# Kernel optimization log

Measured on AMD Instinct MI355X. Metric: run time of the kernel, lower is better.

Reference implementation:

```python
import jax, jax.numpy as jnp
import numpy as np

CHUNK = 32
NUM_HEADS = 4
HEAD_K = 256
HEAD_V = 256
EPS = 1e-05


def l2norm(x, eps=1e-6):
    return x * jax.lax.rsqrt(jnp.sum(x * x, axis=-1, keepdims=True) + eps)


def causal_depthwise_conv(x, w):
    # x: [b, l, d], w: [d, K]; causal depthwise conv1d (left pad K-1)
    K = w.shape[1]
    l = x.shape[1]
    xp = jnp.pad(x, ((0, 0), (K - 1, 0), (0, 0)))
    return sum(w[:, k] * xp[:, k:k + l, :] for k in range(K))


def delta_rule_chunkwise(q, k, v, beta):
    # q,k: [b,h,l,dk], v: [b,h,l,dv], beta: [b,h,l]; l divisible by CHUNK
    b, h, l, dk = q.shape
    dv = v.shape[-1]
    c = CHUNK
    n = l // c
    q = l2norm(q)
    k = l2norm(k)
    v = v * beta[..., None]
    k_beta = k * beta[..., None]
    resh = lambda x: x.reshape(b, h, n, c, x.shape[-1])
    q, k, v, k_beta = map(resh, (q, k, v, k_beta))
    tri_strict = jnp.tril(jnp.ones((c, c), dtype=q.dtype), -1)  # strictly lower
    attn = -(k_beta @ jnp.swapaxes(k, -1, -2)) * tri_strict  # [b,h,n,c,c]

    def body(i, a):
        # a[i, :i] += sum_j a[i, j] * a[j, :i]; zero elsewhere by structure
        row = a[..., i, :]  # [b,h,n,c]
        upd = jnp.einsum('bhnj,bhnjk->bhnk', row, a)
        return a.at[..., i, :].add(upd)

    attn = jax.lax.fori_loop(1, c, body, attn)
    attn = attn + jnp.eye(c, dtype=attn.dtype)
    u = attn @ v        # [b,h,n,c,dv]
    w = attn @ k_beta   # [b,h,n,c,dk]

    mask_causal = jnp.tril(jnp.ones((c, c), dtype=q.dtype), 0)  # incl diag
    S0 = jnp.zeros((b, h, dk, dv), dtype=q.dtype)
    to_front = lambda x: jnp.moveaxis(x, 2, 0)  # [n,b,h,c,d]

    def step(S, inp):
        q_i, k_i, u_i, w_i = inp
        attn_i = (q_i @ jnp.swapaxes(k_i, -1, -2)) * mask_causal
        u_new = u_i - w_i @ S
        o_i = q_i @ S + attn_i @ u_new
        S = S + jnp.swapaxes(k_i, -1, -2) @ u_new
        return S, o_i

    S, o = jax.lax.scan(step, S0, (to_front(q), to_front(k), to_front(u), to_front(w)))
    o = jnp.moveaxis(o, 0, 2).reshape(b, h, l, dv)
    return o, S


def setup_inputs() -> dict:
    key = jax.random.key(0)
    ks = jax.random.split(key, 12)
    b, l, d = 4, 4096, 1024
    sc = 0.02
    return {
        'hidden_states': jax.random.normal(ks[0], (b, l, d), jnp.float32),
        'Wq': jax.random.normal(ks[1], (1024, 1024), jnp.float32) * sc,
        'Wk': jax.random.normal(ks[2], (1024, 1024), jnp.float32) * sc,
        'Wv': jax.random.normal(ks[3], (1024, 1024), jnp.float32) * sc,
        'conv_q': jax.random.normal(ks[4], (1024, 4), jnp.float32) * 0.1,
        'conv_k': jax.random.normal(ks[5], (1024, 4), jnp.float32) * 0.1,
        'conv_v': jax.random.normal(ks[6], (1024, 4), jnp.float32) * 0.1,
        'Wb': jax.random.normal(ks[7], (4, 1024), jnp.float32) * sc,
        'Wmix': jax.random.normal(ks[8], (4, 1024), jnp.float32) * sc,
        'norm_w': jnp.ones((256,), jnp.float32),
        'Wo': jax.random.normal(ks[9], (1024, 1024), jnp.float32) * sc,
    }


def reference(hidden_states, Wq, Wk, Wv, conv_q, conv_k, conv_v, Wb, Wmix, norm_w, Wo):
    x = hidden_states
    b, l, d = x.shape
    h, dk, dv = NUM_HEADS, HEAD_K, HEAD_V
    # projections + depthwise causal short conv + silu
    q = jax.nn.silu(causal_depthwise_conv(x @ Wq.T, conv_q))
    k = jax.nn.silu(causal_depthwise_conv(x @ Wk.T, conv_k))
    v = jax.nn.silu(causal_depthwise_conv(x @ Wv.T, conv_v))
    v_token = v.reshape(b, l, h, dv)
    qh = q.reshape(b, l, h, dk).transpose(0, 2, 1, 3)
    kh = k.reshape(b, l, h, dk).transpose(0, 2, 1, 3)
    vh = v_token.transpose(0, 2, 1, 3)
    beta = jax.nn.sigmoid(x @ Wb.T).transpose(0, 2, 1)  # [b,h,l]
    o, S = delta_rule_chunkwise(qh, kh, vh, beta)
    o = o.transpose(0, 2, 1, 3)  # [b,l,h,dv]
    mix = jax.nn.sigmoid(x @ Wmix.T)[..., None]  # [b,l,h,1]
    o = mix * o + (1.0 - mix) * v_token
    # per-head RMSNorm
    o = o * jax.lax.rsqrt(jnp.mean(o * o, axis=-1, keepdims=True) + EPS) * norm_w
    o = o.reshape(b, l, h * dv) @ Wo.T
    return o
```

## Files before the change

### kernel.cpp

```cpp
#include <hip/hip_runtime.h>
#include <hip/hip_bf16.h>

typedef __hip_bfloat16 bf16;
typedef unsigned short u16;
typedef __attribute__((ext_vector_type(4))) float f32x4;
typedef __attribute__((ext_vector_type(8))) short bf16x8;
typedef __attribute__((ext_vector_type(2))) unsigned int u32x2;

#define MFMA16(a, b, c) __builtin_amdgcn_mfma_f32_16x16x32_bf16((a), (b), (c), 0, 0, 0)

__device__ __forceinline__ float bfu2f(u16 u){
  return __uint_as_float(((unsigned int)u) << 16);
}
__device__ __forceinline__ u16 f2bfu(float x){
  return __builtin_bit_cast(u16, __float2bfloat16(x));
}
__device__ __forceinline__ void gload16(const void* g, const void* l){
  __builtin_amdgcn_global_load_lds(
      (const __attribute__((address_space(1))) unsigned int*)g,
      (__attribute__((address_space(3))) unsigned int*)l, 16, 0, 0);
}

__global__ __launch_bounds__(256) void cvt_bf16(
    const float* __restrict__ src, u16* __restrict__ dst, int n8)
{
  int i = blockIdx.x * 256 + threadIdx.x;
  if (i >= n8) return;
  const float4* s = (const float4*)src;
  float4 a = s[i * 2], b = s[i * 2 + 1];
  u16 o[8] = {f2bfu(a.x), f2bfu(a.y), f2bfu(a.z), f2bfu(a.w),
              f2bfu(b.x), f2bfu(b.y), f2bfu(b.z), f2bfu(b.w)};
  *(bf16x8*)(dst + (size_t)i * 8) = *(bf16x8*)o;
}

__global__ __launch_bounds__(256) void cvt3_bf16(
    const float* __restrict__ s0, const float* __restrict__ s1, const float* __restrict__ s2,
    u16* __restrict__ d0, u16* __restrict__ d1, u16* __restrict__ d2)
{
  const float* s; u16* d;
  if (blockIdx.y == 0)      { s = s0; d = d0; }
  else if (blockIdx.y == 1) { s = s1; d = d1; }
  else                      { s = s2; d = d2; }
  int i = blockIdx.x * 256 + threadIdx.x;
  const float4* sp = (const float4*)s;
  float4 a = sp[i * 2], b = sp[i * 2 + 1];
  u16 o[8] = {f2bfu(a.x), f2bfu(a.y), f2bfu(a.z), f2bfu(a.w),
              f2bfu(b.x), f2bfu(b.y), f2bfu(b.z), f2bfu(b.w)};
  *(bf16x8*)(d + (size_t)i * 8) = *(bf16x8*)o;
}

template<int NMAT, bool F32OUT>
__global__ __launch_bounds__(256) void gemm_bt(
    const u16* __restrict__ A,
    const u16* __restrict__ B0, const u16* __restrict__ B1, const u16* __restrict__ B2,
    void* __restrict__ C0, void* __restrict__ C1, void* __restrict__ C2)
{
  const u16* B; void* C;
  if (NMAT == 1 || blockIdx.z == 0){ B = B0; C = C0; }
  else if (blockIdx.z == 1)        { B = B1; C = C1; }
  else                             { B = B2; C = C2; }
  __shared__ char lds[2][2][16384];
  const int tid = threadIdx.x;
  const int lane = tid & 63, wv = tid >> 6;
  const int lc = lane & 15, lh = lane >> 4;
  const int wr = wv >> 1, wc = wv & 1;
  const int lin = blockIdx.x + (blockIdx.y << 7);
  const int m0 = ((lin & 7) * 16 + (lin >> 6)) * 128;
  const int n0 = ((lin >> 3) & 7) * 128;

  f32x4 acc[4][4];
  #pragma unroll
  for (int mt = 0; mt < 4; mt++)
    #pragma unroll
    for (int nt = 0; nt < 4; nt++) acc[mt][nt] = (f32x4){0.f, 0.f, 0.f, 0.f};

  auto stage = [&](int buf, int k0){
    #pragma unroll
    for (int c = 0; c < 4; c++){
      const int q = wv * 4096 + c * 1024;
      const int row = (q >> 7) + (lane >> 3);
      const int slot = (lane & 7) ^ (row & 7);
      gload16(A + (size_t)(m0 + row) * 1024 + k0 + slot * 8, &lds[buf][0][q]);
      gload16(B + (size_t)(n0 + row) * 1024 + k0 + slot * 8, &lds[buf][1][q]);
    }
  };

  stage(0, 0);
  __syncthreads();
  int cur = 0;
  for (int t = 0; t < 16; t++){
    if (t < 15) stage(cur ^ 1, (t + 1) * 64);
    const char* Abuf = lds[cur][0];
    const char* Bbuf = lds[cur][1];
    #pragma unroll
    for (int kk = 0; kk < 2; kk++){
      bf16x8 af[4], bfr[4];
      #pragma unroll
      for (int mt = 0; mt < 4; mt++){
        int r = wr * 64 + mt * 16 + lc;
        int slot = (kk * 4 + lh) ^ (r & 7);
        af[mt] = *(const bf16x8*)(const void*)(Abuf + r * 128 + slot * 16);
      }
      #pragma unroll
      for (int nt = 0; nt < 4; nt++){
        int r = wc * 64 + nt * 16 + lc;
        int slot = (kk * 4 + lh) ^ (r & 7);
        bfr[nt] = *(const bf16x8*)(const void*)(Bbuf + r * 128 + slot * 16);
      }
      #pragma unroll
      for (int mt = 0; mt < 4; mt++)
        #pragma unroll
        for (int nt = 0; nt < 4; nt++)
          acc[mt][nt] = MFMA16(af[mt], bfr[nt], acc[mt][nt]);
    }
    __syncthreads();
    cur ^= 1;
  }

  #pragma unroll
  for (int mt = 0; mt < 4; mt++)
    #pragma unroll
    for (int nt = 0; nt < 4; nt++)
      #pragma unroll
      for (int rg = 0; rg < 4; rg++){
        int row = m0 + wr * 64 + mt * 16 + lh * 4 + rg;
        int col = n0 + wc * 64 + nt * 16 + lc;
        if (F32OUT) ((float*)C)[(size_t)row * 1024 + col] = acc[mt][nt][rg];
        else ((bf16*)C)[(size_t)row * 1024 + col] = __float2bfloat16(acc[mt][nt][rg]);
      }
}

__global__ __launch_bounds__(256) void small_proj(
    const float* __restrict__ x, const float* __restrict__ Wb,
    const float* __restrict__ Wmix, float* __restrict__ beta, float* __restrict__ mixb)
{
  const int tok = blockIdx.x;
  const int tid = threadIdx.x;
  __shared__ __align__(16) float xrow[1024];
  ((float4*)xrow)[tid] = ((const float4*)(x + (size_t)tok * 1024))[tid];
  __syncthreads();
  const int o = tid >> 5, g = tid & 31;
  const float* Wrow = (o < 4) ? (Wb + (size_t)o * 1024) : (Wmix + (size_t)(o - 4) * 1024);
  float p = 0.f;
  for (int e = g; e < 256; e += 32){
    float4 xv = ((const float4*)xrow)[e];
    float4 wv = ((const float4*)Wrow)[e];
    p += xv.x * wv.x + xv.y * wv.y + xv.z * wv.z + xv.w * wv.w;
  }
  for (int off = 16; off; off >>= 1) p += __shfl_down(p, off, 32);
  if (g == 0){
    float s = 1.f / (1.f + expf(-p));
    int b = tok >> 12, t = tok & 4095;
    if (o < 4) beta[((size_t)(b * 4 + o)) * 4096 + t] = s;
    else       mixb[(size_t)tok * 4 + (o - 4)] = s;
  }
}

__global__ __launch_bounds__(256) void conv_silu3(
    const bf16* __restrict__ in0, const bf16* __restrict__ in1, const bf16* __restrict__ in2,
    const float* __restrict__ w0, const float* __restrict__ w1, const float* __restrict__ w2,
    bf16* __restrict__ o0, bf16* __restrict__ o1, bf16* __restrict__ o2)
{
  const bf16* in; const float* wc; bf16* out;
  if (blockIdx.y == 0)      { in = in0; wc = w0; out = o0; }
  else if (blockIdx.y == 1) { in = in1; wc = w1; out = o1; }
  else                      { in = in2; wc = w2; out = o2; }
  const int idx8 = blockIdx.x * 256 + threadIdx.x;
  const int c8 = (idx8 & 127) * 8;
  const int tt = idx8 >> 7;
  const int t  = tt & 4095;
  const u16* inu = (const u16*)in;
  const size_t base = (size_t)tt * 1024 + c8;
  bf16x8 zv = {0, 0, 0, 0, 0, 0, 0, 0};
  bf16x8 x3 = *(const bf16x8*)(const void*)(inu + base);
  bf16x8 x2 = (t >= 1) ? *(const bf16x8*)(const void*)(inu + base - 1024) : zv;
  bf16x8 x1 = (t >= 2) ? *(const bf16x8*)(const void*)(inu + base - 2048) : zv;
  bf16x8 x0 = (t >= 3) ? *(const bf16x8*)(const void*)(inu + base - 3072) : zv;
  u16 o8[8];
  #pragma unroll
  for (int e = 0; e < 8; e++){
    const float4 w4 = ((const float4*)wc)[c8 + e];
    float s = w4.w * bfu2f((u16)x3[e]) + w4.z * bfu2f((u16)x2[e])
            + w4.y * bfu2f((u16)x1[e]) + w4.x * bfu2f((u16)x0[e]);
    s = s / (1.f + expf(-s));
    o8[e] = f2bfu(s);
  }
  *(bf16x8*)(void*)((u16*)out + base) = *(bf16x8*)o8;
}

__global__ __launch_bounds__(256, 2) void chunk_prep(
    bf16* __restrict__ qc, const bf16* __restrict__ kc, const bf16* __restrict__ vc,
    const float* __restrict__ beta,
    bf16* __restrict__ u_out, bf16* __restrict__ w_out,
    bf16* __restrict__ Ab, bf16* __restrict__ kTg)
{
  __shared__ char kS[16384], qS[16384];
  __shared__ float att[1056];
  __shared__ char Th[2048], Tl[2048];
  __shared__ char vTh[8192], vTl[8192];
  __shared__ char wTh[8192], wTl[8192];
  __shared__ float rnk_s[32], rnq_s[32], bvec[32];

  const int g = blockIdx.x;
  const int ch = g & 127, h = (g >> 7) & 3, b = g >> 9;
  const int tid = threadIdx.x;
  const int l = tid & 63, wv = tid >> 6;
  const int lc = l & 15, lh = l >> 4;
  const int i = tid >> 3, s = tid & 7;
  const size_t rowbase = ((size_t)(b * 4096 + ch * 32)) * 1024 + (size_t)h * 256;
  const u16* kcu = (const u16*)kc;
  const u16* qcu = (const u16*)qc;
  const u16* vcu = (const u16*)vc;

  bf16x8 kr[4], qr[4], vr[4];
  float ssk = 0.f, ssq = 0.f;
  #pragma unroll
  for (int j4 = 0; j4 < 4; j4++){
    size_t eo = rowbase + (size_t)i * 1024 + s * 32 + j4 * 8;
    kr[j4] = *(const bf16x8*)(const void*)(kcu + eo);
    qr[j4] = *(const bf16x8*)(const void*)(qcu + eo);
    vr[j4] = *(const bf16x8*)(const void*)(vcu + eo);
    #pragma unroll
    for (int e = 0; e < 8; e++){
      float kv = bfu2f((u16)kr[j4][e]); ssk += kv * kv;
      float qv = bfu2f((u16)qr[j4][e]); ssq += qv * qv;
    }
  }
  #pragma unroll
  for (int off = 1; off < 8; off <<= 1){
    ssk += __shfl_xor(ssk, off, 64);
    ssq += __shfl_xor(ssq, off, 64);
  }
  if (s == 0){
    rnk_s[i] = 1.0f / sqrtf(ssk + 1e-6f);
    rnq_s[i] = 1.0f / sqrtf(ssq + 1e-6f);
  }
  if (tid < 32) bvec[tid] = beta[((size_t)(b * 4 + h)) * 4096 + ch * 32 + tid];
  __syncthreads();

  const float rk = rnk_s[i], rq = rnq_s[i], bi = bvec[i];
  #pragma unroll
  for (int j4 = 0; j4 < 4; j4++){
    u16 kn8[8], qn8[8];
    #pragma unroll
    for (int e = 0; e < 8; e++){
      kn8[e] = f2bfu(bfu2f((u16)kr[j4][e]) * rk);
      qn8[e] = f2bfu(bfu2f((u16)qr[j4][e]) * rq);
    }
    int byt = (i * 512 + s * 64 + j4 * 16) ^ ((i & 7) << 4);
    *(bf16x8*)(void*)(kS + byt) = *(bf16x8*)kn8;
    *(bf16x8*)(void*)(qS + byt) = *(bf16x8*)qn8;
    *(bf16x8*)(void*)((u16*)qc + rowbase + (size_t)i * 1024 + s * 32 + j4 * 8) = *(bf16x8*)kn8 * 0 + *(bf16x8*)qn8;
  }
  if ((s >> 2) == 0){
    #pragma unroll
    for (int j4 = 0; j4 < 4; j4++)
      #pragma unroll
      for (int e = 0; e < 8; e++){
        int dl = (s & 3) * 32 + j4 * 8 + e;
        float vb = bfu2f((u16)vr[j4][e]) * bi;
        float kb = bfu2f((u16)kr[j4][e]) * rk * bi;
        u16 vh = f2bfu(vb), kh = f2bfu(kb);
        u16 vlo = f2bfu(vb - bfu2f(vh)), klo = f2bfu(kb - bfu2f(kh));
        int byt = dl * 64 + (((i >> 3) ^ ((dl >> 1) & 3)) << 4) + (i & 7) * 2;
        *(u16*)(vTh + byt) = vh; *(u16*)(vTl + byt) = vlo;
        *(u16*)(wTh + byt) = kh; *(u16*)(wTl + byt) = klo;
      }
  }
  __syncthreads();

  {
    const int mq = wv >> 1, nq = wv & 1;
    const int rowA = mq * 16 + lc, rowB = nq * 16 + lc;
    const int swA = (rowA & 7) << 4, swB = (rowB & 7) << 4;
    f32x4 accL = (f32x4){0.f, 0.f, 0.f, 0.f};
    f32x4 accA = (f32x4){0.f, 0.f, 0.f, 0.f};
    #pragma unroll
    for (int kt = 0; kt < 8; kt++){
      bf16x8 af  = *(const bf16x8*)(const void*)(kS + ((rowA * 512 + kt * 64 + lh * 16) ^ swA));
      bf16x8 bf_ = *(const bf16x8*)(const void*)(kS + ((rowB * 512 + kt * 64 + lh * 16) ^ swB));
      bf16x8 aq  = *(const bf16x8*)(const void*)(qS + ((rowA * 512 + kt * 64 + lh * 16) ^ swA));
      accL = MFMA16(af, bf_, accL);
      accA = MFMA16(aq, bf_, accA);
    }
    #pragma unroll
    for (int r = 0; r < 4; r++){
      int rr = mq * 16 + lh * 4 + r, cc = nq * 16 + lc;
      att[rr * 33 + cc] = (cc < rr) ? (-bvec[rr] * accL[r]) : 0.f;
      float av = (cc <= rr) ? accA[r] : 0.f;
      ((u16*)Ab)[(size_t)g * 1024 + rr * 32 + cc] = f2bfu(av);
    }
  }
  {
    u16 tmp[32];
    #pragma unroll
    for (int i2 = 0; i2 < 32; i2++)
      tmp[i2] = *(const u16*)(kS + ((i2 * 512 + tid * 2) ^ ((i2 & 7) << 4)));
    #pragma unroll
    for (int j4 = 0; j4 < 4; j4++)
      *(bf16x8*)(void*)((u16*)kTg + (size_t)g * 8192 + tid * 32 + j4 * 8) = *(bf16x8*)(tmp + j4 * 8);
  }
  __syncthreads();

  if (wv == 0 && l < 32){
    for (int ii = 1; ii < 32; ii++){
      float upd = 0.f;
      for (int m = 0; m < ii; m++)
        upd += att[ii * 33 + m] * att[m * 33 + l];
      att[ii * 33 + l] += upd;
    }
    att[l * 33 + l] = 1.0f;
  }
  __syncthreads();

  #pragma unroll
  for (int z = 0; z < 4; z++){
    int e = tid * 4 + z;
    int row = e >> 5, col = e & 31;
    float f = att[row * 33 + col];
    u16 hh = f2bfu(f), llo = f2bfu(f - bfu2f(hh));
    int byt = row * 64 + ((((col >> 3)) ^ ((row >> 1) & 3)) << 4) + (col & 7) * 2;
    *(u16*)(Th + byt) = hh; *(u16*)(Tl + byt) = llo;
  }
  __syncthreads();

  {
    const int mq = wv >> 1, nsel = wv & 1;
    const int rowA = mq * 16 + lc;
    const int sa = (lh ^ ((rowA >> 1) & 3)) << 4;
    bf16x8 ta = *(const bf16x8*)(const void*)(Th + rowA * 64 + sa);
    bf16x8 tl = *(const bf16x8*)(const void*)(Tl + rowA * 64 + sa);
    #pragma unroll
    for (int half = 0; half < 2; half++){
      if (half == 1){
        __syncthreads();
        if ((s >> 2) == 1){
          #pragma unroll
          for (int j4 = 0; j4 < 4; j4++)
            #pragma unroll
            for (int e = 0; e < 8; e++){
              int dl = (s & 3) * 32 + j4 * 8 + e;
              float vb = bfu2f((u16)vr[j4][e]) * bi;
              float kb = bfu2f((u16)kr[j4][e]) * rk * bi;
              u16 vh = f2bfu(vb), kh = f2bfu(kb);
              u16 vlo = f2bfu(vb - bfu2f(vh)), klo = f2bfu(kb - bfu2f(kh));
              int byt = dl * 64 + (((i >> 3) ^ ((dl >> 1) & 3)) << 4) + (i & 7) * 2;
              *(u16*)(vTh + byt) = vh; *(u16*)(vTl + byt) = vlo;
              *(u16*)(wTh + byt) = kh; *(u16*)(wTl + byt) = klo;
            }
        }
        __syncthreads();
      }
      #pragma unroll
      for (int nt = 0; nt < 4; nt++){
        int nl = nsel * 64 + nt * 16;
        int rowB = nl + lc;
        int sb = (lh ^ ((rowB >> 1) & 3)) << 4;
        bf16x8 bh_ = *(const bf16x8*)(const void*)(vTh + rowB * 64 + sb);
        bf16x8 bl_ = *(const bf16x8*)(const void*)(vTl + rowB * 64 + sb);
        f32x4 aU = (f32x4){0.f, 0.f, 0.f, 0.f};
        aU = MFMA16(ta, bh_, aU);
        aU = MFMA16(ta, bl_, aU);
        aU = MFMA16(tl, bh_, aU);
        bf16x8 wh_ = *(const bf16x8*)(const void*)(wTh + rowB * 64 + sb);
        bf16x8 wl_ = *(const bf16x8*)(const void*)(wTl + rowB * 64 + sb);
        f32x4 aW = (f32x4){0.f, 0.f, 0.f, 0.f};
        aW = MFMA16(ta, wh_, aW);
        aW = MFMA16(ta, wl_, aW);
        aW = MFMA16(tl, wh_, aW);
        #pragma unroll
        for (int r = 0; r < 4; r++){
          int row = mq * 16 + lh * 4 + r, col = half * 128 + nl + lc;
          ((u16*)u_out)[rowbase + (size_t)row * 1024 + col] = f2bfu(aU[r]);
          ((u16*)w_out)[rowbase + (size_t)row * 1024 + col] = f2bfu(aW[r]);
        }
      }
    }
  }
}

__global__ __launch_bounds__(128, 1) void scan_kernel(
    const u16* __restrict__ w_in, const u16* __restrict__ qn,
    const u16* __restrict__ u_in, const bf16* __restrict__ Ab,
    const bf16* __restrict__ kTg, bf16* __restrict__ o_out)
{
  extern __shared__ char smem[];
  char* wqbuf  = smem;
  char* stbuf  = smem + 65536;
  char* untbuf = smem + 81920;

  const int tid = threadIdx.x;
  const int l = tid & 63, wv = tid >> 6;
  const int lc = l & 15, lh = l >> 4;
  const int wg = blockIdx.x;
  const int bh = (wg & 7) * 2 + ((wg >> 3) & 1);
  const int vb = wg >> 4;
  const int h = bh & 3, b = bh >> 2;
  const int c0 = vb * 16;
  const int mw = wv * 16;

  f32x4 Sf[8];
  #pragma unroll
  for (int mt = 0; mt < 8; mt++) Sf[mt] = (f32x4){0.f, 0.f, 0.f, 0.f};

  const size_t bhElem = (size_t)b * 4096 * 1024 + (size_t)h * 256;
  const u16* kTu = (const u16*)kTg;

  auto stageWQ = [&](int buf, size_t rowE){
    char* wbase = wqbuf + buf * 32768 + wv * 8192;
    #pragma unroll
    for (int p = 0; p < 8; p++){
      int i = wv * 16 + p * 2 + (l >> 5);
      int logc = (l & 31) ^ (i & 7);
      size_t src = rowE + (size_t)i * 1024 + (size_t)logc * 8;
      gload16(w_in + src, wbase + p * 1024);
      gload16(qn  + src, wbase + 16384 + p * 1024);
    }
  };

  stageWQ(0, bhElem);
  for (int e = tid; e < 4096; e += 128) ((unsigned int*)(void*)stbuf)[e] = 0u;
  u16 cu0 = u_in[bhElem + (size_t)(mw + lh*4 + 0) * 1024 + c0 + lc];
  u16 cu1 = u_in[bhElem + (size_t)(mw + lh*4 + 1) * 1024 + c0 + lc];
  u16 cu2 = u_in[bhElem + (size_t)(mw + lh*4 + 2) * 1024 + c0 + lc];
  u16 cu3 = u_in[bhElem + (size_t)(mw + lh*4 + 3) * 1024 + c0 + lc];
  bf16x8 cAf = *(const bf16x8*)(const void*)(Ab + (size_t)(bh * 128) * 1024 + (mw + lc) * 32 + lh * 8);
  __syncthreads();

  int cur = 0;
  for (int ch = 0; ch < 128; ch++){
    const size_t rowElem = bhElem + (size_t)ch * 32768;
    if (ch < 127) stageWQ(cur ^ 1, rowElem + 32768);
    bf16x8 kF[8];
    {
      const size_t ktCur = (size_t)(bh * 128 + ch) * 8192;
      #pragma unroll
      for (int mt = 0; mt < 8; mt++){
        int rowK = wv * 128 + mt * 16 + lc;
        kF[mt] = *(const bf16x8*)(const void*)(kTu + ktCur + (size_t)rowK * 32 + lh * 8);
      }
    }
    u16 pu0, pu1, pu2, pu3; bf16x8 pAf;
    if (ch < 127){
      const size_t rowN = rowElem + 32768;
      pu0 = u_in[rowN + (size_t)(mw + lh*4 + 0) * 1024 + c0 + lc];
      pu1 = u_in[rowN + (size_t)(mw + lh*4 + 1) * 1024 + c0 + lc];
      pu2 = u_in[rowN + (size_t)(mw + lh*4 + 2) * 1024 + c0 + lc];
      pu3 = u_in[rowN + (size_t)(mw + lh*4 + 3) * 1024 + c0 + lc];
      pAf = *(const bf16x8*)(const void*)(Ab + (size_t)(bh * 128 + ch + 1) * 1024 + (mw + lc) * 32 + lh * 8);
    }

    const char* wl = wqbuf + cur * 32768;
    const char* ql = wl + 16384;

    f32x4 aU0 = (f32x4){0.f,0.f,0.f,0.f}, aU1 = (f32x4){0.f,0.f,0.f,0.f};
    f32x4 aO0 = (f32x4){0.f,0.f,0.f,0.f}, aO1 = (f32x4){0.f,0.f,0.f,0.f};
    {
      const int rowA = mw + lc;
      const int swA = (rowA & 7) << 4;
      const int swS = (lc & 7) << 4;
      #pragma unroll
      for (int kt = 0; kt < 8; kt++){
        const int kb = kt * 64 + lh * 16;
        bf16x8 aw = *(const bf16x8*)(const void*)(wl + ((rowA * 512 + kb) ^ swA));
        bf16x8 aq = *(const bf16x8*)(const void*)(ql + ((rowA * 512 + kb) ^ swA));
        bf16x8 sh = *(const bf16x8*)(const void*)(stbuf + ((lc * 512 + kb) ^ swS));
        bf16x8 sl = *(const bf16x8*)(const void*)(stbuf + 8192 + ((lc * 512 + kb) ^ swS));
        if (kt & 1){
          aU1 = MFMA16(aw, sh, aU1);
          aU1 = MFMA16(aw, sl, aU1);
          aO1 = MFMA16(aq, sh, aO1);
          aO1 = MFMA16(aq, sl, aO1);
        } else {
          aU0 = MFMA16(aw, sh, aU0);
          aU0 = MFMA16(aw, sl, aU0);
          aO0 = MFMA16(aq, sh, aO0);
          aO0 = MFMA16(aq, sl, aO0);
        }
      }
    }
    f32x4 accO = aO0 + aO1;
    {
      f32x4 accU = aU0 + aU1;
      float v0 = bfu2f(cu0) - accU[0];
      float v1 = bfu2f(cu1) - accU[1];
      float v2 = bfu2f(cu2) - accU[2];
      float v3 = bfu2f(cu3) - accU[3];
      u16 h0 = f2bfu(v0), h1 = f2bfu(v1), h2 = f2bfu(v2), h3 = f2bfu(v3);
      u16 l0 = f2bfu(v0 - bfu2f(h0)), l1 = f2bfu(v1 - bfu2f(h1));
      u16 l2 = f2bfu(v2 - bfu2f(h2)), l3 = f2bfu(v3 - bfu2f(h3));
      unsigned int ph0 = (unsigned)h0 | ((unsigned)h1 << 16), ph1 = (unsigned)h2 | ((unsigned)h3 << 16);
      unsigned int pl0 = (unsigned)l0 | ((unsigned)l1 << 16), pl1 = (unsigned)l2 | ((unsigned)l3 << 16);
      int off = lc * 80 + (mw + lh * 4) * 2;
      *(u32x2*)(void*)(untbuf + off)        = (u32x2){ph0, ph1};
      *(u32x2*)(void*)(untbuf + 1280 + off) = (u32x2){pl0, pl1};
    }
    __syncthreads();

    bf16x8 uh = *(const bf16x8*)(const void*)(untbuf + lc * 80 + lh * 16);
    bf16x8 ul = *(const bf16x8*)(const void*)(untbuf + 1280 + lc * 80 + lh * 16);
    accO = MFMA16(cAf, uh, accO);
    accO = MFMA16(cAf, ul, accO);
    o_out[rowElem + (size_t)(mw + lh*4 + 0) * 1024 + c0 + lc] = __float2bfloat16(accO[0]);
    o_out[rowElem + (size_t)(mw + lh*4 + 1) * 1024 + c0 + lc] = __float2bfloat16(accO[1]);
    o_out[rowElem + (size_t)(mw + lh*4 + 2) * 1024 + c0 + lc] = __float2bfloat16(accO[2]);
    o_out[rowElem + (size_t)(mw + lh*4 + 3) * 1024 + c0 + lc] = __float2bfloat16(accO[3]);

    #pragma unroll
    for (int mt = 0; mt < 8; mt++){
      Sf[mt] = MFMA16(kF[mt], uh, Sf[mt]);
      Sf[mt] = MFMA16(kF[mt], ul, Sf[mt]);
    }

    #pragma unroll
    for (int mt = 0; mt < 8; mt++){
      const int dbase = wv * 128 + mt * 16 + lh * 4;
      float v0 = Sf[mt][0], v1 = Sf[mt][1], v2 = Sf[mt][2], v3 = Sf[mt][3];
      u16 h0 = f2bfu(v0), h1 = f2bfu(v1), h2 = f2bfu(v2), h3 = f2bfu(v3);
      u16 s0 = f2bfu(v0 - bfu2f(h0)), s1 = f2bfu(v1 - bfu2f(h1));
      u16 s2 = f2bfu(v2 - bfu2f(h2)), s3 = f2bfu(v3 - bfu2f(h3));
      int off = ((lc * 512 + dbase * 2) ^ ((lc & 7) << 4));
      *(u32x2*)(void*)(stbuf + off) =
          (u32x2){(unsigned)h0 | ((unsigned)h1 << 16), (unsigned)h2 | ((unsigned)h3 << 16)};
      *(u32x2*)(void*)(stbuf + 8192 + off) =
          (u32x2){(unsigned)s0 | ((unsigned)s1 << 16), (unsigned)s2 | ((unsigned)s3 << 16)};
    }
    if (ch < 127){
      cu0 = pu0; cu1 = pu1; cu2 = pu2; cu3 = pu3; cAf = pAf;
    }
    __syncthreads();
    cur ^= 1;
  }
}

__global__ __launch_bounds__(256) void postproc(
    const bf16* __restrict__ o_in, const bf16* __restrict__ v_tok,
    const float* __restrict__ mixb, const float* __restrict__ norm_w,
    bf16* __restrict__ onorm)
{
  const int tid = threadIdx.x;
  const int slot = tid >> 5, g = tid & 31;
  const int blk = blockIdx.x * 8 + slot;
  const size_t base = (size_t)blk * 256 + g * 8;
  const u16* oin = (const u16*)o_in;
  const u16* vin = (const u16*)v_tok;
  bf16x8 ov8 = *(const bf16x8*)(const void*)(oin + base);
  bf16x8 vv8 = *(const bf16x8*)(const void*)(vin + base);
  float m = mixb[blk];
  float val[8];
  float ss = 0.f;
  #pragma unroll
  for (int e = 0; e < 8; e++){
    float v = m * bfu2f((u16)ov8[e]) + (1.f - m) * bfu2f((u16)vv8[e]);
    val[e] = v;
    ss += v * v;
  }
  #pragma unroll
  for (int off = 16; off; off >>= 1) ss += __shfl_down(ss, off, 32);
  ss = __shfl(ss, 0, 32);
  float r = rsqrtf(ss * (1.f / 256.f) + 1e-5f);
  const float4 nw0 = ((const float4*)norm_w)[g * 2];
  const float4 nw1 = ((const float4*)norm_w)[g * 2 + 1];
  const float nw[8] = {nw0.x, nw0.y, nw0.z, nw0.w, nw1.x, nw1.y, nw1.z, nw1.w};
  u16 o8[8];
  #pragma unroll
  for (int e = 0; e < 8; e++) o8[e] = f2bfu(val[e] * r * nw[e]);
  *(bf16x8*)(void*)((u16*)onorm + base) = *(bf16x8*)o8;
}

extern "C" void kernel_launch(void* const* d_in, const int* in_sizes, int n_in,
                              void* d_out, int out_size, void* d_ws, size_t ws_size,
                              hipStream_t stream)
{
  (void)in_sizes; (void)n_in; (void)out_size; (void)ws_size;
  const float* x     = (const float*)d_in[0];
  const float* Wq    = (const float*)d_in[1];
  const float* Wk    = (const float*)d_in[2];
  const float* Wv    = (const float*)d_in[3];
  const float* convq = (const float*)d_in[4];
  const float* convk = (const float*)d_in[5];
  const float* convv = (const float*)d_in[6];
  const float* Wb    = (const float*)d_in[7];
  const float* Wmix  = (const float*)d_in[8];
  const float* normw = (const float*)d_in[9];
  const float* Wo    = (const float*)d_in[10];
  float* out = (float*)d_out;

  char* wsb = (char*)d_ws;
  const size_t BIGB = (size_t)16777216 * 2;
  bf16* b0 = (bf16*)(wsb + 0*BIGB);
  bf16* b1 = (bf16*)(wsb + 1*BIGB);
  bf16* b2 = (bf16*)(wsb + 2*BIGB);
  bf16* b3 = (bf16*)(wsb + 3*BIGB);
  bf16* b4 = (bf16*)(wsb + 4*BIGB);
  bf16* b5 = (bf16*)(wsb + 5*BIGB);
  bf16*  Ab   = (bf16*) (wsb + 6*BIGB);
  float* beta = (float*)(wsb + 6*BIGB + 4194304);
  float* mixb = beta + 65536;
  bf16*  kTg  = (bf16*) (wsb + 6*BIGB + 4194304 + 524288);

  u16* xbf = (u16*)b4;
  u16* wqb = (u16*)b3;
  u16* wkb = wqb + (size_t)1024*1024;
  u16* wvb = wkb + (size_t)1024*1024;
  u16* wob = (u16*)kTg;

  cvt_bf16<<<8192, 256, 0, stream>>>(x, xbf, 2097152);
  cvt3_bf16<<<dim3(512, 3), 256, 0, stream>>>(Wq, Wk, Wv, wqb, wkb, wvb);

  gemm_bt<3, false><<<dim3(128, 8, 3), 256, 0, stream>>>(
      xbf, wqb, wkb, wvb, (void*)b0, (void*)b1, (void*)b2);
  small_proj<<<16384, 256, 0, stream>>>(x, Wb, Wmix, beta, mixb);
  conv_silu3<<<dim3(8192, 3), 256, 0, stream>>>(
      b0, b1, b2, convq, convk, convv, b3, b4, b5);
  chunk_prep<<<2048, 256, 0, stream>>>(b3, b4, b5, beta, b2, b0, Ab, kTg);
  hipFuncSetAttribute((const void*)scan_kernel,
                      hipFuncAttributeMaxDynamicSharedMemorySize, 84480);
  scan_kernel<<<256, 128, 84480, stream>>>((const u16*)b0, (const u16*)b3,
                                           (const u16*)b2, Ab, kTg, b1);
  cvt_bf16<<<512, 256, 0, stream>>>(Wo, wob, 131072);
  postproc  <<<8192, 256, 0, stream>>>(b1, b5, mixb, normw, b3);
  gemm_bt<1, true><<<dim3(128, 8, 1), 256, 0, stream>>>(
      (const u16*)b3, wob, wob, wob, (void*)out, (void*)out, (void*)out);
}
```

Measured before the change: 626.2 us.

## Process chunk pairs in scan with precomputed cross-chunk correction matrices

```diff
diff --git a/kernel.cpp b/kernel.cpp
--- a/kernel.cpp
+++ b/kernel.cpp
@@ -379,10 +379,69 @@
   }
 }
 
+__global__ __launch_bounds__(256) void pair_prep(
+    const u16* __restrict__ w_in, const u16* __restrict__ qn,
+    const bf16* __restrict__ kTg, u16* __restrict__ MN)
+{
+  __shared__ char wS[16384], qS[16384], ktS[16384];
+  const int g2 = blockIdx.x;
+  const int bh = g2 >> 6, p = g2 & 63;
+  const int h = bh & 3, b = bh >> 2;
+  const int tid = threadIdx.x;
+  const int l = tid & 63, wv = tid >> 6;
+  const int lc = l & 15, lh = l >> 4;
+  const int i = tid >> 3, s = tid & 7;
+  const size_t row1 = ((size_t)(b * 4096 + (p * 2 + 1) * 32)) * 1024 + (size_t)h * 256;
+  const u16* kt0 = (const u16*)kTg + (size_t)(bh * 128 + p * 2) * 8192;
+
+  #pragma unroll
+  for (int j4 = 0; j4 < 4; j4++){
+    size_t eo = row1 + (size_t)i * 1024 + s * 32 + j4 * 8;
+    int byt = (i * 512 + s * 64 + j4 * 16) ^ ((i & 7) << 4);
+    *(bf16x8*)(void*)(wS + byt) = *(const bf16x8*)(const void*)(w_in + eo);
+    *(bf16x8*)(void*)(qS + byt) = *(const bf16x8*)(const void*)(qn + eo);
+  }
+  #pragma unroll
+  for (int j = 0; j < 4; j++)
+    *(bf16x8*)(void*)(ktS + tid * 64 + j * 16) = *(const bf16x8*)(const void*)(kt0 + tid * 32 + j * 8);
+  __syncthreads();
+
+  const int mq = wv >> 1, nq = wv & 1;
+  const int rowA = mq * 16 + lc;
+  const int swA = (rowA & 7) << 4;
+  f32x4 accM = (f32x4){0.f, 0.f, 0.f, 0.f};
+  f32x4 accN = (f32x4){0.f, 0.f, 0.f, 0.f};
+  #pragma unroll
+  for (int kt = 0; kt < 8; kt++){
+    bf16x8 aw = *(const bf16x8*)(const void*)(wS + ((rowA * 512 + kt * 64 + lh * 16) ^ swA));
+    bf16x8 aq = *(const bf16x8*)(const void*)(qS + ((rowA * 512 + kt * 64 + lh * 16) ^ swA));
+    u16 bk8[8];
+    #pragma unroll
+    for (int j = 0; j < 8; j++)
+      bk8[j] = *(const u16*)(ktS + (kt * 32 + lh * 8 + j) * 64 + (nq * 16 + lc) * 2);
+    bf16x8 bk = *(bf16x8*)bk8;
+    accM = MFMA16(aw, bk, accM);
+    accN = MFMA16(aq, bk, accN);
+  }
+  u16* base = MN + (size_t)g2 * 4096;
+  #pragma unroll
+  for (int r = 0; r < 4; r++){
+    int rr = mq * 16 + lh * 4 + r, cc = nq * 16 + lc;
+    float m = accM[r], n = accN[r];
+    u16 mh = f2bfu(m), nh = f2bfu(n);
+    u16 ml = f2bfu(m - bfu2f(mh)), nl = f2bfu(n - bfu2f(nh));
+    base[rr * 32 + cc] = mh;
+    base[1024 + rr * 32 + cc] = ml;
+    base[2048 + rr * 32 + cc] = nh;
+    base[3072 + rr * 32 + cc] = nl;
+  }
+}
+
 __global__ __launch_bounds__(128, 1) void scan_kernel(
     const u16* __restrict__ w_in, const u16* __restrict__ qn,
     const u16* __restrict__ u_in, const bf16* __restrict__ Ab,
-    const bf16* __restrict__ kTg, bf16* __restrict__ o_out)
+    const bf16* __restrict__ kTg, const u16* __restrict__ MN,
+    bf16* __restrict__ o_out)
 {
   extern __shared__ char smem[];
   char* wqbuf  = smem;
@@ -409,56 +468,67 @@
   auto stageWQ = [&](int buf, size_t rowE){
     char* wbase = wqbuf + buf * 32768 + wv * 8192;
     #pragma unroll
-    for (int p = 0; p < 8; p++){
-      int i = wv * 16 + p * 2 + (l >> 5);
+    for (int pp = 0; pp < 8; pp++){
+      int i = wv * 16 + pp * 2 + (l >> 5);
       int logc = (l & 31) ^ (i & 7);
       size_t src = rowE + (size_t)i * 1024 + (size_t)logc * 8;
-      gload16(w_in + src, wbase + p * 1024);
-      gload16(qn  + src, wbase + 16384 + p * 1024);
+      gload16(w_in + src, wbase + pp * 1024);
+      gload16(qn  + src, wbase + 16384 + pp * 1024);
     }
   };
 
   stageWQ(0, bhElem);
   for (int e = tid; e < 4096; e += 128) ((unsigned int*)(void*)stbuf)[e] = 0u;
-  u16 cu0 = u_in[bhElem + (size_t)(mw + lh*4 + 0) * 1024 + c0 + lc];
-  u16 cu1 = u_in[bhElem + (size_t)(mw + lh*4 + 1) * 1024 + c0 + lc];
-  u16 cu2 = u_in[bhElem + (size_t)(mw + lh*4 + 2) * 1024 + c0 + lc];
-  u16 cu3 = u_in[bhElem + (size_t)(mw + lh*4 + 3) * 1024 + c0 + lc];
-  bf16x8 cAf = *(const bf16x8*)(const void*)(Ab + (size_t)(bh * 128) * 1024 + (mw + lc) * 32 + lh * 8);
   __syncthreads();
 
   int cur = 0;
-  for (int ch = 0; ch < 128; ch++){
-    const size_t rowElem = bhElem + (size_t)ch * 32768;
-    if (ch < 127) stageWQ(cur ^ 1, rowElem + 32768);
-    bf16x8 kF[8];
+  for (int p = 0; p < 64; p++){
+    const size_t row0 = bhElem + (size_t)(p * 2) * 32768;
+    const size_t row1 = row0 + 32768;
+    if (p < 63) stageWQ(cur ^ 1, row0 + 65536);
+
+    bf16x8 w1f[8], q1f[8];
     {
-      const size_t ktCur = (size_t)(bh * 128 + ch) * 8192;
+      const size_t rowOff1 = row1 + (size_t)(mw + lc) * 1024 + lh * 8;
+      #pragma unroll
+      for (int kt = 0; kt < 8; kt++){
+        w1f[kt] = *(const bf16x8*)(const void*)(w_in + rowOff1 + kt * 32);
+        q1f[kt] = *(const bf16x8*)(const void*)(qn + rowOff1 + kt * 32);
+      }
+    }
+    bf16x8 kF0[8], kF1[8];
+    {
+      const size_t kt0b = (size_t)(bh * 128 + p * 2) * 8192;
       #pragma unroll
       for (int mt = 0; mt < 8; mt++){
         int rowK = wv * 128 + mt * 16 + lc;
-        kF[mt] = *(const bf16x8*)(const void*)(kTu + ktCur + (size_t)rowK * 32 + lh * 8);
-      }
-    }
-    u16 pu0, pu1, pu2, pu3; bf16x8 pAf;
-    if (ch < 127){
-      const size_t rowN = rowElem + 32768;
-      pu0 = u_in[rowN + (size_t)(mw + lh*4 + 0) * 1024 + c0 + lc];
-      pu1 = u_in[rowN + (size_t)(mw + lh*4 + 1) * 1024 + c0 + lc];
-      pu2 = u_in[rowN + (size_t)(mw + lh*4 + 2) * 1024 + c0 + lc];
-      pu3 = u_in[rowN + (size_t)(mw + lh*4 + 3) * 1024 + c0 + lc];
-      pAf = *(const bf16x8*)(const void*)(Ab + (size_t)(bh * 128 + ch + 1) * 1024 + (mw + lc) * 32 + lh * 8);
-    }
+        kF0[mt] = *(const bf16x8*)(const void*)(kTu + kt0b + (size_t)rowK * 32 + lh * 8);
+        kF1[mt] = *(const bf16x8*)(const void*)(kTu + kt0b + 8192 + (size_t)rowK * 32 + lh * 8);
+      }
+    }
+    u16 u0v[4], u1v[4];
+    #pragma unroll
+    for (int r = 0; r < 4; r++){
+      u0v[r] = u_in[row0 + (size_t)(mw + lh*4 + r) * 1024 + c0 + lc];
+      u1v[r] = u_in[row1 + (size_t)(mw + lh*4 + r) * 1024 + c0 + lc];
+    }
+    bf16x8 A0f = *(const bf16x8*)(const void*)(Ab + (size_t)(bh * 128 + p * 2) * 1024 + (mw + lc) * 32 + lh * 8);
+    bf16x8 A1f = *(const bf16x8*)(const void*)(Ab + (size_t)(bh * 128 + p * 2 + 1) * 1024 + (mw + lc) * 32 + lh * 8);
+    const u16* mnb = MN + (size_t)(bh * 64 + p) * 4096;
+    bf16x8 Mhf = *(const bf16x8*)(const void*)(mnb + (mw + lc) * 32 + lh * 8);
+    bf16x8 Mlf = *(const bf16x8*)(const void*)(mnb + 1024 + (mw + lc) * 32 + lh * 8);
+    bf16x8 Nhf = *(const bf16x8*)(const void*)(mnb + 2048 + (mw + lc) * 32 + lh * 8);
+    bf16x8 Nlf = *(const bf16x8*)(const void*)(mnb + 3072 + (mw + lc) * 32 + lh * 8);
 
     const char* wl = wqbuf + cur * 32768;
     const char* ql = wl + 16384;
+    const int swS = (lc & 7) << 4;
 
     f32x4 aU0 = (f32x4){0.f,0.f,0.f,0.f}, aU1 = (f32x4){0.f,0.f,0.f,0.f};
     f32x4 aO0 = (f32x4){0.f,0.f,0.f,0.f}, aO1 = (f32x4){0.f,0.f,0.f,0.f};
     {
       const int rowA = mw + lc;
       const int swA = (rowA & 7) << 4;
-      const int swS = (lc & 7) << 4;
       #pragma unroll
       for (int kt = 0; kt < 8; kt++){
         const int kb = kt * 64 + lh * 16;
@@ -467,49 +537,97 @@
         bf16x8 sh = *(const bf16x8*)(const void*)(stbuf + ((lc * 512 + kb) ^ swS));
         bf16x8 sl = *(const bf16x8*)(const void*)(stbuf + 8192 + ((lc * 512 + kb) ^ swS));
         if (kt & 1){
-          aU1 = MFMA16(aw, sh, aU1);
-          aU1 = MFMA16(aw, sl, aU1);
-          aO1 = MFMA16(aq, sh, aO1);
-          aO1 = MFMA16(aq, sl, aO1);
+          aU1 = MFMA16(aw, sh, aU1); aU1 = MFMA16(aw, sl, aU1);
+          aO1 = MFMA16(aq, sh, aO1); aO1 = MFMA16(aq, sl, aO1);
         } else {
-          aU0 = MFMA16(aw, sh, aU0);
-          aU0 = MFMA16(aw, sl, aU0);
-          aO0 = MFMA16(aq, sh, aO0);
-          aO0 = MFMA16(aq, sl, aO0);
+          aU0 = MFMA16(aw, sh, aU0); aU0 = MFMA16(aw, sl, aU0);
+          aO0 = MFMA16(aq, sh, aO0); aO0 = MFMA16(aq, sl, aO0);
         }
       }
     }
-    f32x4 accO = aO0 + aO1;
+    f32x4 accO0 = aO0 + aO1;
     {
-      f32x4 accU = aU0 + aU1;
-      float v0 = bfu2f(cu0) - accU[0];
-      float v1 = bfu2f(cu1) - accU[1];
-      float v2 = bfu2f(cu2) - accU[2];
-      float v3 = bfu2f(cu3) - accU[3];
+      f32x4 accU0 = aU0 + aU1;
+      float v0 = bfu2f(u0v[0]) - accU0[0];
+      float v1 = bfu2f(u0v[1]) - accU0[1];
+      float v2 = bfu2f(u0v[2]) - accU0[2];
+      float v3 = bfu2f(u0v[3]) - accU0[3];
       u16 h0 = f2bfu(v0), h1 = f2bfu(v1), h2 = f2bfu(v2), h3 = f2bfu(v3);
       u16 l0 = f2bfu(v0 - bfu2f(h0)), l1 = f2bfu(v1 - bfu2f(h1));
       u16 l2 = f2bfu(v2 - bfu2f(h2)), l3 = f2bfu(v3 - bfu2f(h3));
-      unsigned int ph0 = (unsigned)h0 | ((unsigned)h1 << 16), ph1 = (unsigned)h2 | ((unsigned)h3 << 16);
-      unsigned int pl0 = (unsigned)l0 | ((unsigned)l1 << 16), pl1 = (unsigned)l2 | ((unsigned)l3 << 16);
       int off = lc * 80 + (mw + lh * 4) * 2;
-      *(u32x2*)(void*)(untbuf + off)        = (u32x2){ph0, ph1};
-      *(u32x2*)(void*)(untbuf + 1280 + off) = (u32x2){pl0, pl1};
+      *(u32x2*)(void*)(untbuf + off) =
+          (u32x2){(unsigned)h0 | ((unsigned)h1 << 16), (unsigned)h2 | ((unsigned)h3 << 16)};
+      *(u32x2*)(void*)(untbuf + 1280 + off) =
+          (u32x2){(unsigned)l0 | ((unsigned)l1 << 16), (unsigned)l2 | ((unsigned)l3 << 16)};
     }
     __syncthreads();
 
-    bf16x8 uh = *(const bf16x8*)(const void*)(untbuf + lc * 80 + lh * 16);
-    bf16x8 ul = *(const bf16x8*)(const void*)(untbuf + 1280 + lc * 80 + lh * 16);
-    accO = MFMA16(cAf, uh, accO);
-    accO = MFMA16(cAf, ul, accO);
-    o_out[rowElem + (size_t)(mw + lh*4 + 0) * 1024 + c0 + lc] = __float2bfloat16(accO[0]);
-    o_out[rowElem + (size_t)(mw + lh*4 + 1) * 1024 + c0 + lc] = __float2bfloat16(accO[1]);
-    o_out[rowElem + (size_t)(mw + lh*4 + 2) * 1024 + c0 + lc] = __float2bfloat16(accO[2]);
-    o_out[rowElem + (size_t)(mw + lh*4 + 3) * 1024 + c0 + lc] = __float2bfloat16(accO[3]);
-
+    bf16x8 uh0 = *(const bf16x8*)(const void*)(untbuf + lc * 80 + lh * 16);
+    bf16x8 ul0 = *(const bf16x8*)(const void*)(untbuf + 1280 + lc * 80 + lh * 16);
+    accO0 = MFMA16(A0f, uh0, accO0);
+    accO0 = MFMA16(A0f, ul0, accO0);
+    #pragma unroll
+    for (int r = 0; r < 4; r++)
+      o_out[row0 + (size_t)(mw + lh*4 + r) * 1024 + c0 + lc] = __float2bfloat16(accO0[r]);
     #pragma unroll
     for (int mt = 0; mt < 8; mt++){
-      Sf[mt] = MFMA16(kF[mt], uh, Sf[mt]);
-      Sf[mt] = MFMA16(kF[mt], ul, Sf[mt]);
+      Sf[mt] = MFMA16(kF0[mt], uh0, Sf[mt]);
+      Sf[mt] = MFMA16(kF0[mt], ul0, Sf[mt]);
+    }
+
+    f32x4 bU0 = (f32x4){0.f,0.f,0.f,0.f}, bU1 = (f32x4){0.f,0.f,0.f,0.f};
+    f32x4 bO0 = (f32x4){0.f,0.f,0.f,0.f}, bO1 = (f32x4){0.f,0.f,0.f,0.f};
+    {
+      #pragma unroll
+      for (int kt = 0; kt < 8; kt++){
+        const int kb = kt * 64 + lh * 16;
+        bf16x8 sh = *(const bf16x8*)(const void*)(stbuf + ((lc * 512 + kb) ^ swS));
+        bf16x8 sl = *(const bf16x8*)(const void*)(stbuf + 8192 + ((lc * 512 + kb) ^ swS));
+        if (kt & 1){
+          bU1 = MFMA16(w1f[kt], sh, bU1); bU1 = MFMA16(w1f[kt], sl, bU1);
+          bO1 = MFMA16(q1f[kt], sh, bO1); bO1 = MFMA16(q1f[kt], sl, bO1);
+        } else {
+          bU0 = MFMA16(w1f[kt], sh, bU0); bU0 = MFMA16(w1f[kt], sl, bU0);
+          bO0 = MFMA16(q1f[kt], sh, bO0); bO0 = MFMA16(q1f[kt], sl, bO0);
+        }
+      }
+    }
+    f32x4 accU1 = bU0 + bU1;
+    f32x4 accO1 = bO0 + bO1;
+    accU1 = MFMA16(Mhf, uh0, accU1);
+    accU1 = MFMA16(Mhf, ul0, accU1);
+    accU1 = MFMA16(Mlf, uh0, accU1);
+    accO1 = MFMA16(Nhf, uh0, accO1);
+    accO1 = MFMA16(Nhf, ul0, accO1);
+    accO1 = MFMA16(Nlf, uh0, accO1);
+    {
+      float v0 = bfu2f(u1v[0]) - accU1[0];
+      float v1 = bfu2f(u1v[1]) - accU1[1];
+      float v2 = bfu2f(u1v[2]) - accU1[2];
+      float v3 = bfu2f(u1v[3]) - accU1[3];
+      u16 h0 = f2bfu(v0), h1 = f2bfu(v1), h2 = f2bfu(v2), h3 = f2bfu(v3);
+      u16 l0 = f2bfu(v0 - bfu2f(h0)), l1 = f2bfu(v1 - bfu2f(h1));
+      u16 l2 = f2bfu(v2 - bfu2f(h2)), l3 = f2bfu(v3 - bfu2f(h3));
+      int off = lc * 80 + (mw + lh * 4) * 2;
+      *(u32x2*)(void*)(untbuf + 2560 + off) =
+          (u32x2){(unsigned)h0 | ((unsigned)h1 << 16), (unsigned)h2 | ((unsigned)h3 << 16)};
+      *(u32x2*)(void*)(untbuf + 3840 + off) =
+          (u32x2){(unsigned)l0 | ((unsigned)l1 << 16), (unsigned)l2 | ((unsigned)l3 << 16)};
+    }
+    __syncthreads();
+
+    bf16x8 uh1 = *(const bf16x8*)(const void*)(untbuf + 2560 + lc * 80 + lh * 16);
+    bf16x8 ul1 = *(const bf16x8*)(const void*)(untbuf + 3840 + lc * 80 + lh * 16);
+    accO1 = MFMA16(A1f, uh1, accO1);
+    accO1 = MFMA16(A1f, ul1, accO1);
+    #pragma unroll
+    for (int r = 0; r < 4; r++)
+      o_out[row1 + (size_t)(mw + lh*4 + r) * 1024 + c0 + lc] = __float2bfloat16(accO1[r]);
+    #pragma unroll
+    for (int mt = 0; mt < 8; mt++){
+      Sf[mt] = MFMA16(kF1[mt], uh1, Sf[mt]);
+      Sf[mt] = MFMA16(kF1[mt], ul1, Sf[mt]);
     }
 
     #pragma unroll
@@ -524,9 +642,6 @@
           (u32x2){(unsigned)h0 | ((unsigned)h1 << 16), (unsigned)h2 | ((unsigned)h3 << 16)};
       *(u32x2*)(void*)(stbuf + 8192 + off) =
           (u32x2){(unsigned)s0 | ((unsigned)s1 << 16), (unsigned)s2 | ((unsigned)s3 << 16)};
-    }
-    if (ch < 127){
-      cu0 = pu0; cu1 = pu1; cu2 = pu2; cu3 = pu3; cAf = pAf;
     }
     __syncthreads();
     cur ^= 1;
@@ -598,6 +713,7 @@
   float* beta = (float*)(wsb + 6*BIGB + 4194304);
   float* mixb = beta + 65536;
   bf16*  kTg  = (bf16*) (wsb + 6*BIGB + 4194304 + 524288);
+  u16*   MN   = (u16*)  (wsb + 6*BIGB + 4194304 + 524288 + 33554432);
 
   u16* xbf = (u16*)b4;
   u16* wqb = (u16*)b3;
@@ -614,10 +730,11 @@
   conv_silu3<<<dim3(8192, 3), 256, 0, stream>>>(
       b0, b1, b2, convq, convk, convv, b3, b4, b5);
   chunk_prep<<<2048, 256, 0, stream>>>(b3, b4, b5, beta, b2, b0, Ab, kTg);
+  pair_prep<<<1024, 256, 0, stream>>>((const u16*)b0, (const u16*)b3, kTg, MN);
   hipFuncSetAttribute((const void*)scan_kernel,
-                      hipFuncAttributeMaxDynamicSharedMemorySize, 84480);
-  scan_kernel<<<256, 128, 84480, stream>>>((const u16*)b0, (const u16*)b3,
-                                           (const u16*)b2, Ab, kTg, b1);
+                      hipFuncAttributeMaxDynamicSharedMemorySize, 87040);
+  scan_kernel<<<256, 128, 87040, stream>>>((const u16*)b0, (const u16*)b3,
+                                           (const u16*)b2, Ab, kTg, MN, b1);
   cvt_bf16<<<512, 256, 0, stream>>>(Wo, wob, 131072);
   postproc  <<<8192, 256, 0, stream>>>(b1, b5, mixb, normw, b3);
   gemm_bt<1, true><<<dim3(128, 8, 1), 256, 0, stream>>>(
```

Measured after the change: 642.9 us. 1.03x slower.
